# Optimization experiments

Measured on AMD Instinct MI355X. Metric: run time of the kernel, lower is better.

The kernel has to match this reference:

```python
import jax, jax.numpy as jnp
import numpy as np

NEG_BIG = 1e30  # matches the 1e+30 masking constant in the original


def setup_inputs() -> dict:
    key = jax.random.key(0)
    ks = jax.random.split(key, 6)
    B, Lc, Lq, D = 8, 512, 64, 256
    return {
        "context": jax.random.normal(ks[0], (B, Lc, D), jnp.float32),
        "question": jax.random.normal(ks[1], (B, Lq, D), jnp.float32),
        "mask": jnp.ones((B, Lq), jnp.int32),
        "att_w": jax.random.normal(ks[2], (3 * D,), jnp.float32) * 0.05,  # Linear(6H=3D -> 1) weight
        "att_b": jnp.zeros((1,), jnp.float32),                            # Linear bias
        "w_in": jax.random.normal(ks[3], (D,), jnp.float32) * 0.05,       # input_linear (no bias)
        "w_mem": jax.random.normal(ks[4], (D,), jnp.float32) * 0.05,      # memory_linear (no bias)
    }


def reference(context, question, mask, att_w, att_b, w_in, w_mem):
    # context: [B,Lc,D], question: [B,Lq,D], mask: [B,Lq] (0/1)
    D = context.shape[-1]
    # Separable (mathematically identical) form of Linear(cat([c, q, c*q])):
    # score[b,i,j] = c_i . w_c + q_j . w_q + sum_d c[b,i,d]*q[b,j,d]*w_p[d] + b
    w_c, w_q, w_p = att_w[:D], att_w[D:2 * D], att_w[2 * D:]
    sc = jnp.einsum('bid,d->bi', context, w_c)                 # [B,Lc]
    sq = jnp.einsum('bjd,d->bj', question, w_q)                # [B,Lq]
    sp = jnp.einsum('bid,bjd->bij', context * w_p, question)   # [B,Lc,Lq]
    attention = sc[:, :, None] + sq[:, None, :] + sp + att_b[0]

    maskf = mask.astype(attention.dtype)
    masked = attention - NEG_BIG * (1.0 - maskf)[:, None, :]   # [B,Lc,Lq]

    ctx1 = jnp.einsum('bid,d->bi', context, w_in)[..., None]   # input_linear:  [B,Lc,1]
    q1 = jnp.einsum('bjd,d->bj', question, w_mem)[..., None]   # memory_linear: [B,Lq,1]

    h_aware_weight = jax.nn.softmax(masked, axis=-1)           # [B,Lc,Lq]
    U = jnp.matmul(h_aware_weight, q1)                         # [B,Lc,1]

    u_aware_weight = jax.nn.softmax(jnp.max(masked, axis=-1), axis=-1)[:, None, :]  # [B,1,Lc]
    H = jnp.matmul(u_aware_weight, ctx1)                       # [B,1,1]

    G = jnp.concatenate([ctx1, U, ctx1 * U, U * H], axis=-1)   # [B,Lc,4]
    return G
```

## Files before the change

### kernel.cpp

```cpp
#include <hip/hip_runtime.h>

#define NB 8
#define LC 512
#define LQ 64
#define DD 256
#define NEG_BIG_F 1e30f

#define TPB 512
#define NWAVE 8
#define RPW 2
#define RPB (NWAVE * RPW)
#define BPB (LC / RPB)

__device__ __forceinline__ float bcastf(float x, int lane) {
  return __uint_as_float((unsigned)__builtin_amdgcn_readlane((int)__float_as_uint(x), lane));
}

__global__ __launch_bounds__(TPB, 2) void rows_kernel(
    const float* __restrict__ context,
    const float* __restrict__ question,
    const int*   __restrict__ mask,
    const float* __restrict__ att_w,
    const float* __restrict__ att_b,
    const float* __restrict__ w_in,
    const float* __restrict__ w_mem,
    float4* __restrict__ ws4)
{
  __shared__ float4 T[64][64];
  __shared__ float sq_raw[LQ];
  __shared__ float q1_s[LQ];

  const int tid  = threadIdx.x;
  const int w    = tid >> 6;
  const int l    = tid & 63;
  const int b    = blockIdx.x / BPB;
  const int row0 = (blockIdx.x % BPB) * RPB;
  const int iA   = row0 + w * RPW;
  const int iB   = iA + 1;

  const float4 wc4 = ((const float4*)att_w)[l];
  const float4 wq4 = ((const float4*)(att_w + DD))[l];
  const float4 wp4 = ((const float4*)(att_w + 2 * DD))[l];
  const float4 wi4 = ((const float4*)w_in)[l];
  const float4 wm4 = ((const float4*)w_mem)[l];
  const float4 cA  = ((const float4*)(context + ((size_t)b * LC + iA) * DD))[l];
  const float4 cB  = ((const float4*)(context + ((size_t)b * LC + iB) * DD))[l];

  float4 v[8];
#pragma unroll
  for (int k = 0; k < 8; ++k)
    v[k] = ((const float4*)(question + ((size_t)b * LQ + (k * 8 + w)) * DD))[l];
#pragma unroll
  for (int k = 0; k < 8; ++k)
    T[l][(k * 8 + w) ^ (l & 7)] = v[k];

  float psq[8], pq1[8];
#pragma unroll
  for (int k = 0; k < 8; ++k) {
    psq[k] = v[k].x*wq4.x + v[k].y*wq4.y + v[k].z*wq4.z + v[k].w*wq4.w;
    pq1[k] = v[k].x*wm4.x + v[k].y*wm4.y + v[k].z*wm4.z + v[k].w*wm4.w;
  }
#pragma unroll
  for (int off = 32; off > 0; off >>= 1) {
#pragma unroll
    for (int k = 0; k < 8; ++k) {
      psq[k] += __shfl_xor(psq[k], off);
      pq1[k] += __shfl_xor(pq1[k], off);
    }
  }
  if (l == 0) {
#pragma unroll
    for (int k = 0; k < 8; ++k) {
      sq_raw[k * 8 + w] = psq[k];
      q1_s[k * 8 + w]   = pq1[k];
    }
  }

  float4 cpA, cpB;
  cpA.x = cA.x*wp4.x; cpA.y = cA.y*wp4.y; cpA.z = cA.z*wp4.z; cpA.w = cA.w*wp4.w;
  cpB.x = cB.x*wp4.x; cpB.y = cB.y*wp4.y; cpB.z = cB.z*wp4.z; cpB.w = cB.w*wp4.w;
  float scA = cA.x*wc4.x + cA.y*wc4.y + cA.z*wc4.z + cA.w*wc4.w;
  float scB = cB.x*wc4.x + cB.y*wc4.y + cB.z*wc4.z + cB.w*wc4.w;
  float c1A = cA.x*wi4.x + cA.y*wi4.y + cA.z*wi4.z + cA.w*wi4.w;
  float c1B = cB.x*wi4.x + cB.y*wi4.y + cB.z*wi4.z + cB.w*wi4.w;
#pragma unroll
  for (int off = 32; off > 0; off >>= 1) {
    scA += __shfl_xor(scA, off);
    scB += __shfl_xor(scB, off);
    c1A += __shfl_xor(c1A, off);
    c1B += __shfl_xor(c1B, off);
  }

  __syncthreads();

  float a0 = 0.f, a1 = 0.f, a2 = 0.f, a3 = 0.f;
  float e0 = 0.f, e1 = 0.f, e2 = 0.f, e3 = 0.f;
#pragma unroll
  for (int c = 0; c < 64; ++c) {
    float4 qv = T[c][l ^ (c & 7)];
    a0 += bcastf(cpA.x, c) * qv.x;
    a1 += bcastf(cpA.y, c) * qv.y;
    a2 += bcastf(cpA.z, c) * qv.z;
    a3 += bcastf(cpA.w, c) * qv.w;
    e0 += bcastf(cpB.x, c) * qv.x;
    e1 += bcastf(cpB.y, c) * qv.y;
    e2 += bcastf(cpB.z, c) * qv.z;
    e3 += bcastf(cpB.w, c) * qv.w;
  }

  const float mf   = (float)mask[b * LQ + l];
  const float base = sq_raw[l] + att_b[0] - NEG_BIG_F * (1.0f - mf);
  float sA = (a0 + a1) + (a2 + a3) + scA + base;
  float sB = (e0 + e1) + (e2 + e3) + scB + base;
  const float q1_l = q1_s[l];

  float mA = sA, mB = sB;
#pragma unroll
  for (int off = 32; off > 0; off >>= 1) {
    mA = fmaxf(mA, __shfl_xor(mA, off));
    mB = fmaxf(mB, __shfl_xor(mB, off));
  }
  float pA = __expf(sA - mA);
  float pB = __expf(sB - mB);
  float psA = pA, puA = pA * q1_l;
  float psB = pB, puB = pB * q1_l;
#pragma unroll
  for (int off = 32; off > 0; off >>= 1) {
    psA += __shfl_xor(psA, off);
    puA += __shfl_xor(puA, off);
    psB += __shfl_xor(psB, off);
    puB += __shfl_xor(puB, off);
  }
  if (l == 0) {
    ws4[b * LC + iA] = make_float4(mA, c1A, puA / psA, 0.f);
    ws4[b * LC + iB] = make_float4(mB, c1B, puB / psB, 0.f);
  }
}

__global__ __launch_bounds__(512) void batch_kernel(
    const float4* __restrict__ ws4,
    float4* __restrict__ out4)
{
  const int b  = blockIdx.x;
  const int t  = threadIdx.x;
  const int gi = b * LC + t;
  const float4 v = ws4[gi];
  const float m = v.x, c1 = v.y, U = v.z;

  const int w = t >> 6, l = t & 63;
  __shared__ float rmax[8], rs[8], rc[8];

  float mx = m;
#pragma unroll
  for (int off = 32; off > 0; off >>= 1) mx = fmaxf(mx, __shfl_xor(mx, off));
  if (l == 0) rmax[w] = mx;
  __syncthreads();
  mx = rmax[0];
#pragma unroll
  for (int k = 1; k < 8; ++k) mx = fmaxf(mx, rmax[k]);

  float p  = __expf(m - mx);
  float ps = p;
  float pc = p * c1;
#pragma unroll
  for (int off = 32; off > 0; off >>= 1) {
    ps += __shfl_xor(ps, off);
    pc += __shfl_xor(pc, off);
  }
  if (l == 0) { rs[w] = ps; rc[w] = pc; }
  __syncthreads();
  float S = 0.f, C = 0.f;
#pragma unroll
  for (int k = 0; k < 8; ++k) { S += rs[k]; C += rc[k]; }

  const float H = C / S;
  out4[gi] = make_float4(c1, U, c1 * U, U * H);
}

extern "C" void kernel_launch(void* const* d_in, const int* in_sizes, int n_in,
                              void* d_out, int out_size, void* d_ws, size_t ws_size,
                              hipStream_t stream) {
  const float* context  = (const float*)d_in[0];
  const float* question = (const float*)d_in[1];
  const int*   mask     = (const int*)d_in[2];
  const float* att_w    = (const float*)d_in[3];
  const float* att_b    = (const float*)d_in[4];
  const float* w_in     = (const float*)d_in[5];
  const float* w_mem    = (const float*)d_in[6];
  float4* out4 = (float4*)d_out;
  float4* ws4  = (float4*)d_ws;

  rows_kernel<<<dim3(NB * BPB), dim3(TPB), 0, stream>>>(
      context, question, mask, att_w, att_b, w_in, w_mem, ws4);
  batch_kernel<<<dim3(NB), dim3(512), 0, stream>>>(ws4, out4);
}
```

Baseline: 76.34 us.

## Fuse per-batch softmax reduction into rows kernel via last-block atomic counter

Merges the second batch-reduction kernel into the rows kernel. Each block bumps a per-batch atomic counter after writing its row results, and the last block to finish for that batch does the cross-row softmax and writes the output. This removes one kernel launch and its launch gap. In exchange it adds threadfences, an atomic per block and a hipMemsetAsync to reset the counters, which is itself an extra stream operation.

Result: slower. 110.9 us (+45.3%).

```diff
diff --git a/kernel.cpp b/kernel.cpp
--- a/kernel.cpp
+++ b/kernel.cpp
@@ -11,12 +11,13 @@
 #define RPW 2
 #define RPB (NWAVE * RPW)
 #define BPB (LC / RPB)
+#define CNT_OFF (NB * LC * 16)
 
 __device__ __forceinline__ float bcastf(float x, int lane) {
   return __uint_as_float((unsigned)__builtin_amdgcn_readlane((int)__float_as_uint(x), lane));
 }
 
-__global__ __launch_bounds__(TPB, 2) void rows_kernel(
+__global__ __launch_bounds__(TPB, 2) void fused_kernel(
     const float* __restrict__ context,
     const float* __restrict__ question,
     const int*   __restrict__ mask,
@@ -24,11 +25,15 @@
     const float* __restrict__ att_b,
     const float* __restrict__ w_in,
     const float* __restrict__ w_mem,
-    float4* __restrict__ ws4)
+    float4* __restrict__ ws4,
+    int*    __restrict__ cnt,
+    float4* __restrict__ out4)
 {
   __shared__ float4 T[64][64];
   __shared__ float sq_raw[LQ];
   __shared__ float q1_s[LQ];
+  __shared__ float rr[3][NWAVE];
+  __shared__ int   lastv;
 
   const int tid  = threadIdx.x;
   const int w    = tid >> 6;
@@ -135,46 +140,44 @@
     ws4[b * LC + iA] = make_float4(mA, c1A, puA / psA, 0.f);
     ws4[b * LC + iB] = make_float4(mB, c1B, puB / psB, 0.f);
   }
-}
-
-__global__ __launch_bounds__(512) void batch_kernel(
-    const float4* __restrict__ ws4,
-    float4* __restrict__ out4)
-{
-  const int b  = blockIdx.x;
-  const int t  = threadIdx.x;
-  const int gi = b * LC + t;
-  const float4 v = ws4[gi];
-  const float m = v.x, c1 = v.y, U = v.z;
-
-  const int w = t >> 6, l = t & 63;
-  __shared__ float rmax[8], rs[8], rc[8];
-
-  float mx = m;
+
+  __threadfence();
+  __syncthreads();
+  if (tid == 0) {
+    const int old = atomicAdd(&cnt[b], 1);
+    lastv = (old == BPB - 1);
+  }
+  __syncthreads();
+  if (!lastv) return;
+  if (tid == 0) __threadfence();
+  __syncthreads();
+
+  const float4 vA = ws4[b * LC + tid];
+  float mx = vA.x;
 #pragma unroll
   for (int off = 32; off > 0; off >>= 1) mx = fmaxf(mx, __shfl_xor(mx, off));
-  if (l == 0) rmax[w] = mx;
-  __syncthreads();
-  mx = rmax[0];
-#pragma unroll
-  for (int k = 1; k < 8; ++k) mx = fmaxf(mx, rmax[k]);
-
-  float p  = __expf(m - mx);
-  float ps = p;
-  float pc = p * c1;
-#pragma unroll
-  for (int off = 32; off > 0; off >>= 1) {
-    ps += __shfl_xor(ps, off);
-    pc += __shfl_xor(pc, off);
-  }
-  if (l == 0) { rs[w] = ps; rc[w] = pc; }
-  __syncthreads();
-  float S = 0.f, C = 0.f;
-#pragma unroll
-  for (int k = 0; k < 8; ++k) { S += rs[k]; C += rc[k]; }
-
+  if (l == 0) rr[0][w] = mx;
+  __syncthreads();
+  mx = rr[0][0];
+#pragma unroll
+  for (int k = 1; k < NWAVE; ++k) mx = fmaxf(mx, rr[0][k]);
+
+  const float p = __expf(vA.x - mx);
+  float S = p;
+  float C = p * vA.y;
+#pragma unroll
+  for (int off = 32; off > 0; off >>= 1) {
+    S += __shfl_xor(S, off);
+    C += __shfl_xor(C, off);
+  }
+  if (l == 0) { rr[1][w] = S; rr[2][w] = C; }
+  __syncthreads();
+  S = 0.f; C = 0.f;
+#pragma unroll
+  for (int k = 0; k < NWAVE; ++k) { S += rr[1][k]; C += rr[2][k]; }
   const float H = C / S;
-  out4[gi] = make_float4(c1, U, c1 * U, U * H);
+
+  out4[b * LC + tid] = make_float4(vA.y, vA.z, vA.y * vA.z, vA.z * H);
 }
 
 extern "C" void kernel_launch(void* const* d_in, const int* in_sizes, int n_in,
@@ -189,8 +192,10 @@
   const float* w_mem    = (const float*)d_in[6];
   float4* out4 = (float4*)d_out;
   float4* ws4  = (float4*)d_ws;
-
-  rows_kernel<<<dim3(NB * BPB), dim3(TPB), 0, stream>>>(
-      context, question, mask, att_w, att_b, w_in, w_mem, ws4);
-  batch_kernel<<<dim3(NB), dim3(512), 0, stream>>>(ws4, out4);
+  int*    cnt  = (int*)((char*)d_ws + CNT_OFF);
+
+  hipMemsetAsync(cnt, 0, NB * sizeof(int), stream);
+
+  fused_kernel<<<dim3(NB * BPB), dim3(TPB), 0, stream>>>(
+      context, question, mask, att_w, att_b, w_in, w_mem, ws4, cnt, out4);
 }
```
